# Optimization experiments

Measured on AMD Instinct MI355X. Metric: run time of the kernel, lower is better.

## Reference

```python
import jax, jax.numpy as jnp
import numpy as np

B, S = 1024, 256
E, EU = 8, 1            # total experts, universal experts
ES = E - EU             # specialized experts
UW = 0.3                # universal_expert_weight
NSTEPS = 1001
COV = 512
H = 128
DATA_DIM = 2


def setup_inputs() -> dict:
    key = jax.random.key(0)
    ks = iter(jax.random.split(key, 64))

    def nrm(shape, s=0.02):
        return jax.random.normal(next(ks), shape, jnp.float32) * s

    inp = {
        "y_t": jax.random.normal(next(ks), (B, S, 1), jnp.float32),
        "y_0_hat": jax.random.normal(next(ks), (B, S, 1), jnp.float32),
        "cov_embedding": jax.random.normal(next(ks), (B, COV), jnp.float32),
        "t": jax.random.randint(next(ks), (B,), 0, NSTEPS),
    }
    for l, nin in zip((1, 2, 3), (DATA_DIM, H, H)):
        inp[f"l{l}_emb"] = jax.random.uniform(next(ks), (NSTEPS, H), jnp.float32)  # embed.weight.uniform_()
        inp[f"l{l}_W"] = nrm((E, nin, H))      # per-expert Linear weights
        inp[f"l{l}_b"] = jnp.zeros((E, H), jnp.float32)
        inp[f"l{l}_Wc"] = nrm((COV, H))        # cov_projection
        inp[f"l{l}_bc"] = jnp.zeros((H,), jnp.float32)
        inp[f"l{l}_Wr1"] = nrm((COV, COV // 2))  # specialized_router layer 1
        inp[f"l{l}_br1"] = jnp.zeros((COV // 2,), jnp.float32)
        inp[f"l{l}_Wr2"] = nrm((COV // 2, ES))   # specialized_router layer 2
        inp[f"l{l}_br2"] = jnp.zeros((ES,), jnp.float32)
    inp["W4"] = nrm((H, 1))
    inp["b4"] = jnp.zeros((1,), jnp.float32)
    return inp


def _moe_layer(x, t, cov, emb, W, b, Wc, bc, Wr1, br1, Wr2, br2):
    # x: [B,S,in]; t: [B] int; cov: [B,COV]
    gamma = emb[t][:, None, :]                                   # [B,1,H]
    hr = jax.nn.relu(cov @ Wr1 + br1)                            # router (dropout inactive in eval)
    rw = jax.nn.softmax(hr @ Wr2 + br2, axis=-1) * (1.0 - UW)    # [B,ES] specialized routing weights
    w = jnp.concatenate(
        [jnp.full((x.shape[0], EU), UW / EU, x.dtype), rw], axis=1
    )                                                            # [B,E] full routing weights
    # gamma factors out of the weighted sum over experts, so fuse expert GEMMs + weighting:
    mix = jnp.einsum('bsi,eio,be->bso', x, W, w) + jnp.einsum('be,eo->bo', w, b)[:, None, :]
    mix = gamma * mix
    cov_gamma = cov @ Wc + bc                                    # [B,H]
    mix = mix * (1.0 + cov_gamma[:, None, :])
    usage = rw.mean(axis=0)                                      # mean over batch
    load = jnp.mean((usage - 1.0 / ES) ** 2)                     # mse vs uniform
    return mix, load


def reference(y_t, y_0_hat, cov_embedding, t,
              l1_emb, l1_W, l1_b, l1_Wc, l1_bc, l1_Wr1, l1_br1, l1_Wr2, l1_br2,
              l2_emb, l2_W, l2_b, l2_Wc, l2_bc, l2_Wr1, l2_br1, l2_Wr2, l2_br2,
              l3_emb, l3_W, l3_b, l3_Wc, l3_bc, l3_Wr1, l3_br1, l3_Wr2, l3_br2,
              W4, b4):
    h = jnp.concatenate([y_t, y_0_hat], axis=-1)                 # cat_y_pred: [B,S,2]
    h, ld1 = _moe_layer(h, t, cov_embedding, l1_emb, l1_W, l1_b, l1_Wc, l1_bc, l1_Wr1, l1_br1, l1_Wr2, l1_br2)
    h = jax.nn.softplus(h)
    h, ld2 = _moe_layer(h, t, cov_embedding, l2_emb, l2_W, l2_b, l2_Wc, l2_bc, l2_Wr1, l2_br1, l2_Wr2, l2_br2)
    h = jax.nn.softplus(h)
    h, ld3 = _moe_layer(h, t, cov_embedding, l3_emb, l3_W, l3_b, l3_Wc, l3_bc, l3_Wr1, l3_br1, l3_Wr2, l3_br2)
    h = jax.nn.softplus(h)
    out = h @ W4 + b4                                            # [B,S,1] velocity
    return out, ld1 + ld2 + ld3
```

## Files before the change

kernel.cpp:

```cpp
#include <hip/hip_runtime.h>
#include <hip/hip_bf16.h>
#include <math.h>

#define B_    1024
#define S_    256
#define COV_  512
#define H_    128
#define E_    8
#define ES_   7

#define W_WS_OFF   0
#define COVG_OFF   24576
#define USAGE_OFF  417792

#define AT_STRIDE  136
#define WT_STRIDE  40

typedef __attribute__((ext_vector_type(8))) short bf16x8;
typedef __attribute__((ext_vector_type(4))) float f32x4;

__device__ __forceinline__ float softplus_f(float x) {
    return fmaxf(x, 0.0f) + __logf(1.0f + __expf(-fabsf(x)));
}

__device__ __forceinline__ unsigned pk2_bf16(float a, float b) {
    __hip_bfloat162 h = __float22bfloat162_rn(make_float2(a, b));
    return *reinterpret_cast<unsigned*>(&h);
}
__device__ __forceinline__ void split_pair(float a, float b, unsigned &hi, unsigned &lo) {
    hi = pk2_bf16(a, b);
    float ha = __uint_as_float(hi << 16);
    float hb = __uint_as_float(hi & 0xffff0000u);
    lo = pk2_bf16(a - ha, b - hb);
}

struct RouterArgs {
    const float* cov;
    const float* Wr1[3];
    const float* br1[3];
    const float* Wr2[3];
    const float* br2[3];
    const float* Wc[3];
    const float* bc[3];
    float* ws;
};

__global__ __launch_bounds__(384) void router_kernel(RouterArgs a) {
    const int l   = blockIdx.y;
    const int b0  = blockIdx.x * 4;
    const int tid = threadIdx.x;

    __shared__ float4 covs[4][COV_ / 4];
    __shared__ float  hr[4][256];
    __shared__ float  susage[ES_];

    for (int f = tid; f < 512; f += 384) {
        const int bb = f >> 7, k4 = f & 127;
        covs[bb][k4] = ((const float4*)(a.cov + (size_t)(b0 + bb) * COV_))[k4];
    }
    if (tid < ES_) susage[tid] = 0.0f;
    __syncthreads();

    {
        const float* __restrict__ Wp;
        int stride; float bias;
        if (tid < 256) { Wp = a.Wr1[l] + tid;         stride = 256; bias = a.br1[l][tid]; }
        else           { Wp = a.Wc[l]  + (tid - 256); stride = 128; bias = a.bc[l][tid - 256]; }

        float acc[4] = {0.f, 0.f, 0.f, 0.f};
        #pragma unroll 4
        for (int k4 = 0; k4 < COV_ / 4; ++k4) {
            float w0 = Wp[(4 * k4 + 0) * stride];
            float w1 = Wp[(4 * k4 + 1) * stride];
            float w2 = Wp[(4 * k4 + 2) * stride];
            float w3 = Wp[(4 * k4 + 3) * stride];
            #pragma unroll
            for (int bb = 0; bb < 4; ++bb) {
                float4 c = covs[bb][k4];
                acc[bb] = fmaf(c.x, w0, acc[bb]);
                acc[bb] = fmaf(c.y, w1, acc[bb]);
                acc[bb] = fmaf(c.z, w2, acc[bb]);
                acc[bb] = fmaf(c.w, w3, acc[bb]);
            }
        }
        if (tid < 256) {
            #pragma unroll
            for (int bb = 0; bb < 4; ++bb)
                hr[bb][tid] = fmaxf(acc[bb] + bias, 0.0f);
        } else {
            #pragma unroll
            for (int bb = 0; bb < 4; ++bb)
                a.ws[COVG_OFF + (size_t)(l * B_ + b0 + bb) * H_ + (tid - 256)] = acc[bb] + bias;
        }
    }
    __syncthreads();

    {
        const int wave = tid >> 6;
        const int lane = tid & 63;
        if (wave < 4) {
            const int bb = wave;
            const int o = lane >> 3;
            const int g = lane & 7;
            float p = 0.0f;
            if (o < ES_) {
                #pragma unroll
                for (int m = 0; m < 32; ++m) {
                    const int k = g * 32 + m;
                    p = fmaf(hr[bb][k], a.Wr2[l][k * ES_ + o], p);
                }
            }
            p += __shfl_xor(p, 1);
            p += __shfl_xor(p, 2);
            p += __shfl_xor(p, 4);
            const float lg = p + ((o < ES_) ? a.br2[l][o] : 0.0f);
            float v[ES_];
            #pragma unroll
            for (int oo = 0; oo < ES_; ++oo) v[oo] = __shfl(lg, oo * 8, 64);
            if (lane == 0) {
                const int b = b0 + bb;
                float mx = v[0];
                #pragma unroll
                for (int oo = 1; oo < ES_; ++oo) mx = fmaxf(mx, v[oo]);
                float ex[ES_]; float s = 0.0f;
                #pragma unroll
                for (int oo = 0; oo < ES_; ++oo) { ex[oo] = __expf(v[oo] - mx); s += ex[oo]; }
                const float inv = 0.7f / s;
                float* wout = a.ws + W_WS_OFF + (size_t)(l * B_ + b) * 8;
                wout[0] = 0.3f;
                #pragma unroll
                for (int oo = 0; oo < ES_; ++oo) {
                    const float rwv = ex[oo] * inv;
                    wout[1 + oo] = rwv;
                    atomicAdd(&susage[oo], rwv);
                }
            }
        }
    }
    __syncthreads();
    if (tid < ES_) atomicAdd(a.ws + USAGE_OFF + l * ES_ + tid, susage[tid]);
}

struct MainArgs {
    const float* y_t;
    const float* y0;
    const int*   t;
    const float* emb[3];
    const float* W1;
    const float* W2;
    const float* W3;
    const float* b_[3];
    const float* W4;
    const float* b4;
    float* ws;
    float* out;
};

__global__ __launch_bounds__(512, 2) void main_kernel(MainArgs a) {
    __shared__ unsigned short Ahi[256 * AT_STRIDE];
    __shared__ unsigned short Alo[256 * AT_STRIDE];
    __shared__ unsigned short WtBuf[2][128 * WT_STRIDE];
    __shared__ float GPs[2][128];
    __shared__ float GPBs[2][128];
    __shared__ float W4s[128];

    const int tid  = threadIdx.x;
    const int b    = blockIdx.x;
    const int lane = tid & 63;
    const int w    = tid >> 6;
    const int wm   = w >> 1;
    const int wn   = w & 1;
    const int nl   = lane & 15;
    const int quad = lane >> 4;
    const int tb   = a.t[b];

    float* L1f = (float*)WtBuf;

    if (tid < 384) {
        const int l = tid >> 7, j = tid & 127;
        const float* wv = a.ws + W_WS_OFF + (size_t)(l * B_ + b) * 8;
        const float gamma = a.emb[l][tb * H_ + j];
        const float covg  = a.ws[COVG_OFF + (size_t)(l * B_ + b) * H_ + j];
        const float gp = gamma * (1.0f + covg);
        const float* bl = a.b_[l];
        float bm = 0.0f;
        #pragma unroll
        for (int e = 0; e < E_; ++e) bm = fmaf(wv[e], bl[e * H_ + j], bm);
        if (l == 0) {
            float s0 = 0.0f, s1 = 0.0f;
            #pragma unroll
            for (int e = 0; e < E_; ++e) {
                s0 = fmaf(wv[e], a.W1[e * 256 + j], s0);
                s1 = fmaf(wv[e], a.W1[e * 256 + 128 + j], s1);
            }
            L1f[j]       = gp * s0;
            L1f[128 + j] = gp * s1;
            L1f[256 + j] = gp * bm;
        } else {
            GPs[l - 1][j]  = gp;
            GPBs[l - 1][j] = gp * bm;
        }
    }
    if (tid < 128) W4s[tid] = a.W4[tid];
    __syncthreads();

    {
        const int tok = tid >> 1;
        const int jh  = (tid & 1) * 64;
        const float x0 = a.y_t[b * S_ + tok];
        const float x1 = a.y0[b * S_ + tok];
        #pragma unroll
        for (int g = 0; g < 8; ++g) {
            const int jb = jh + g * 8;
            unsigned hp[4], lp[4];
            #pragma unroll
            for (int p = 0; p < 4; ++p) {
                const int j0 = jb + 2 * p;
                float m0 = fmaf(x0, L1f[j0],     fmaf(x1, L1f[128 + j0],     L1f[256 + j0]));
                float m1 = fmaf(x0, L1f[j0 + 1], fmaf(x1, L1f[128 + j0 + 1], L1f[256 + j0 + 1]));
                split_pair(softplus_f(m0), softplus_f(m1), hp[p], lp[p]);
            }
            *(uint4*)&Ahi[tok * AT_STRIDE + jb] = make_uint4(hp[0], hp[1], hp[2], hp[3]);
            *(uint4*)&Alo[tok * AT_STRIDE + jb] = make_uint4(lp[0], lp[1], lp[2], lp[3]);
        }
    }

    const int bj  = tid & 127;
    const int bkg = tid >> 7;

    for (int L = 0; L < 2; ++L) {
        const float* __restrict__ Wg = L ? a.W3 : a.W2;
        const float* wv = a.ws + W_WS_OFF + (size_t)((L + 1) * B_ + b) * 8;
        float we[E_];
        #pragma unroll
        for (int e = 0; e < E_; ++e) we[e] = wv[e];

        f32x4 acc[4][4];
        #pragma unroll
        for (int mt = 0; mt < 4; ++mt)
            #pragma unroll
            for (int nt = 0; nt < 4; ++nt)
                acc[mt][nt] = (f32x4){0.f, 0.f, 0.f, 0.f};

        unsigned bh[4], blo_[4];
        auto build = [&](int kc) {
            float bacc[8] = {0,0,0,0,0,0,0,0};
            const float* base = Wg + (size_t)(kc * 32 + bkg * 8) * H_ + bj;
            #pragma unroll
            for (int e = 0; e < E_; ++e) {
                const float* p = base + (size_t)e * (H_ * H_);
                const float wE = we[e];
                #pragma unroll
                for (int i = 0; i < 8; ++i)
                    bacc[i] = fmaf(wE, p[i * H_], bacc[i]);
            }
            #pragma unroll
            for (int i = 0; i < 4; ++i)
                split_pair(bacc[2 * i], bacc[2 * i + 1], bh[i], blo_[i]);
        };

        build(0);

        for (int kc = 0; kc < 4; ++kc) {
            __syncthreads();
            *(uint4*)&WtBuf[0][bj * WT_STRIDE + bkg * 8] = make_uint4(bh[0], bh[1], bh[2], bh[3]);
            *(uint4*)&WtBuf[1][bj * WT_STRIDE + bkg * 8] = make_uint4(blo_[0], blo_[1], blo_[2], blo_[3]);
            __syncthreads();

            const int ka = kc * 32 + quad * 8;
            bf16x8 Af[4], Al[4], Bf[4], Bl[4];
            #pragma unroll
            for (int mt = 0; mt < 4; ++mt) {
                const int row = (wm * 64 + mt * 16 + nl) * AT_STRIDE + ka;
                Af[mt] = *(const bf16x8*)&Ahi[row];
                Al[mt] = *(const bf16x8*)&Alo[row];
            }
            #pragma unroll
            for (int nt = 0; nt < 4; ++nt) {
                const int row = (wn * 64 + nt * 16 + nl) * WT_STRIDE + quad * 8;
                Bf[nt] = *(const bf16x8*)&WtBuf[0][row];
                Bl[nt] = *(const bf16x8*)&WtBuf[1][row];
            }
            #pragma unroll
            for (int mt = 0; mt < 4; ++mt)
                #pragma unroll
                for (int nt = 0; nt < 4; ++nt) {
                    acc[mt][nt] = __builtin_amdgcn_mfma_f32_16x16x32_bf16(Af[mt], Bf[nt], acc[mt][nt], 0, 0, 0);
                    acc[mt][nt] = __builtin_amdgcn_mfma_f32_16x16x32_bf16(Af[mt], Bl[nt], acc[mt][nt], 0, 0, 0);
                    acc[mt][nt] = __builtin_amdgcn_mfma_f32_16x16x32_bf16(Al[mt], Bf[nt], acc[mt][nt], 0, 0, 0);
                }

            if (kc < 3) build(kc + 1);
        }
        __syncthreads();

        if (L == 0) {
            #pragma unroll
            for (int nt = 0; nt < 4; ++nt) {
                const int n = wn * 64 + nt * 16 + nl;
                const float gp = GPs[0][n], gpb = GPBs[0][n];
                #pragma unroll
                for (int mt = 0; mt < 4; ++mt) {
                    const int tok0 = wm * 64 + mt * 16 + quad * 4;
                    #pragma unroll
                    for (int rp = 0; rp < 2; ++rp) {
                        const float h0 = softplus_f(fmaf(gp, acc[mt][nt][2 * rp],     gpb));
                        const float h1 = softplus_f(fmaf(gp, acc[mt][nt][2 * rp + 1], gpb));
                        unsigned hh, ll;
                        split_pair(h0, h1, hh, ll);
                        const int t0 = tok0 + 2 * rp;
                        Ahi[t0 * AT_STRIDE + n]       = (unsigned short)hh;
                        Ahi[(t0 + 1) * AT_STRIDE + n] = (unsigned short)(hh >> 16);
                        Alo[t0 * AT_STRIDE + n]       = (unsigned short)ll;
                        Alo[(t0 + 1) * AT_STRIDE + n] = (unsigned short)(ll >> 16);
                    }
                }
            }
        } else {
            float po[4][4];
            #pragma unroll
            for (int mt = 0; mt < 4; ++mt)
                #pragma unroll
                for (int r = 0; r < 4; ++r) po[mt][r] = 0.0f;
            #pragma unroll
            for (int nt = 0; nt < 4; ++nt) {
                const int n = wn * 64 + nt * 16 + nl;
                const float gp = GPs[1][n], gpb = GPBs[1][n], w4 = W4s[n];
                #pragma unroll
                for (int mt = 0; mt < 4; ++mt)
                    #pragma unroll
                    for (int r = 0; r < 4; ++r) {
                        const float h = softplus_f(fmaf(gp, acc[mt][nt][r], gpb));
                        po[mt][r] = fmaf(h, w4, po[mt][r]);
                    }
            }
            #pragma unroll
            for (int mt = 0; mt < 4; ++mt)
                #pragma unroll
                for (int r = 0; r < 4; ++r) {
                    po[mt][r] += __shfl_xor(po[mt][r], 1);
                    po[mt][r] += __shfl_xor(po[mt][r], 2);
                    po[mt][r] += __shfl_xor(po[mt][r], 4);
                    po[mt][r] += __shfl_xor(po[mt][r], 8);
                }
            float* pos = (float*)WtBuf;
            if (nl == 0) {
                #pragma unroll
                for (int mt = 0; mt < 4; ++mt)
                    #pragma unroll
                    for (int r = 0; r < 4; ++r)
                        pos[(wm * 64 + mt * 16 + quad * 4 + r) * 2 + wn] = po[mt][r];
            }
            __syncthreads();
            if (tid < 256)
                a.out[b * S_ + tid] = pos[2 * tid] + pos[2 * tid + 1] + a.b4[0];
        }
    }

    if (b == 0 && tid == 0) {
        float ld = 0.0f;
        for (int l = 0; l < 3; ++l)
            for (int o = 0; o < ES_; ++o) {
                float u = a.ws[USAGE_OFF + l * ES_ + o] * (1.0f / (float)B_);
                float d = u - (1.0f / (float)ES_);
                ld = fmaf(d, d, ld);
            }
        a.out[B_ * S_] = ld * (1.0f / (float)ES_);
    }
}

extern "C" void kernel_launch(void* const* d_in, const int* in_sizes, int n_in,
                              void* d_out, int out_size, void* d_ws, size_t ws_size,
                              hipStream_t stream) {
    (void)in_sizes; (void)n_in; (void)out_size; (void)ws_size;

    RouterArgs ra;
    ra.cov = (const float*)d_in[2];
    ra.ws  = (float*)d_ws;

    MainArgs ma;
    ma.y_t = (const float*)d_in[0];
    ma.y0  = (const float*)d_in[1];
    ma.t   = (const int*)d_in[3];
    for (int l = 0; l < 3; ++l) {
        const int base = 4 + l * 9;
        ma.emb[l] = (const float*)d_in[base + 0];
        ma.b_[l]  = (const float*)d_in[base + 2];
        ra.Wc[l]  = (const float*)d_in[base + 3];
        ra.bc[l]  = (const float*)d_in[base + 4];
        ra.Wr1[l] = (const float*)d_in[base + 5];
        ra.br1[l] = (const float*)d_in[base + 6];
        ra.Wr2[l] = (const float*)d_in[base + 7];
        ra.br2[l] = (const float*)d_in[base + 8];
    }
    ma.W1 = (const float*)d_in[4 + 0 * 9 + 1];
    ma.W2 = (const float*)d_in[4 + 1 * 9 + 1];
    ma.W3 = (const float*)d_in[4 + 2 * 9 + 1];
    ma.W4 = (const float*)d_in[31];
    ma.b4 = (const float*)d_in[32];
    ma.ws  = (float*)d_ws;
    ma.out = (float*)d_out;

    (void)hipMemsetAsync((char*)d_ws + USAGE_OFF * sizeof(float), 0, 24 * sizeof(float), stream);
    router_kernel<<<dim3(256, 3, 1), 384, 0, stream>>>(ra);
    main_kernel<<<dim3(1024, 1, 1), 512, 0, stream>>>(ma);
}
```

Baseline: 322.5 us.

## Double main-kernel threads per block and read router cov directly

The main kernel now launches 1024 threads per block instead of 512. Each wave takes half as many token rows in the MFMA tiles, and the weight-build and layer-1 work are split more finely across threads. This aims to put more waves on each CU to hide latency, since LDS use already limits the kernel to about one block per CU. The launch bound of (1024, 4) may force a very low VGPR cap and cause register spills. Separately, the router kernel drops its shared-memory staging of the covariance rows and reads them directly from global memory inside the K loop, which removes one barrier but relies on caching for reuse.

```diff
diff --git a/kernel.cpp b/kernel.cpp
--- a/kernel.cpp
+++ b/kernel.cpp
@@ -50,16 +50,14 @@
     const int b0  = blockIdx.x * 4;
     const int tid = threadIdx.x;
 
-    __shared__ float4 covs[4][COV_ / 4];
-    __shared__ float  hr[4][256];
-    __shared__ float  susage[ES_];
-
-    for (int f = tid; f < 512; f += 384) {
-        const int bb = f >> 7, k4 = f & 127;
-        covs[bb][k4] = ((const float4*)(a.cov + (size_t)(b0 + bb) * COV_))[k4];
-    }
+    __shared__ float hr[4][256];
+    __shared__ float susage[ES_];
     if (tid < ES_) susage[tid] = 0.0f;
-    __syncthreads();
+
+    const float* __restrict__ c0 = a.cov + (size_t)(b0 + 0) * COV_;
+    const float* __restrict__ c1 = a.cov + (size_t)(b0 + 1) * COV_;
+    const float* __restrict__ c2 = a.cov + (size_t)(b0 + 2) * COV_;
+    const float* __restrict__ c3 = a.cov + (size_t)(b0 + 3) * COV_;
 
     {
         const float* __restrict__ Wp;
@@ -67,30 +65,26 @@
         if (tid < 256) { Wp = a.Wr1[l] + tid;         stride = 256; bias = a.br1[l][tid]; }
         else           { Wp = a.Wc[l]  + (tid - 256); stride = 128; bias = a.bc[l][tid - 256]; }
 
-        float acc[4] = {0.f, 0.f, 0.f, 0.f};
-        #pragma unroll 4
-        for (int k4 = 0; k4 < COV_ / 4; ++k4) {
-            float w0 = Wp[(4 * k4 + 0) * stride];
-            float w1 = Wp[(4 * k4 + 1) * stride];
-            float w2 = Wp[(4 * k4 + 2) * stride];
-            float w3 = Wp[(4 * k4 + 3) * stride];
-            #pragma unroll
-            for (int bb = 0; bb < 4; ++bb) {
-                float4 c = covs[bb][k4];
-                acc[bb] = fmaf(c.x, w0, acc[bb]);
-                acc[bb] = fmaf(c.y, w1, acc[bb]);
-                acc[bb] = fmaf(c.z, w2, acc[bb]);
-                acc[bb] = fmaf(c.w, w3, acc[bb]);
-            }
+        float acc0 = 0.f, acc1 = 0.f, acc2 = 0.f, acc3 = 0.f;
+        #pragma unroll 8
+        for (int k = 0; k < COV_; ++k) {
+            const float wv = Wp[(size_t)k * stride];
+            acc0 = fmaf(c0[k], wv, acc0);
+            acc1 = fmaf(c1[k], wv, acc1);
+            acc2 = fmaf(c2[k], wv, acc2);
+            acc3 = fmaf(c3[k], wv, acc3);
         }
         if (tid < 256) {
-            #pragma unroll
-            for (int bb = 0; bb < 4; ++bb)
-                hr[bb][tid] = fmaxf(acc[bb] + bias, 0.0f);
+            hr[0][tid] = fmaxf(acc0 + bias, 0.0f);
+            hr[1][tid] = fmaxf(acc1 + bias, 0.0f);
+            hr[2][tid] = fmaxf(acc2 + bias, 0.0f);
+            hr[3][tid] = fmaxf(acc3 + bias, 0.0f);
         } else {
-            #pragma unroll
-            for (int bb = 0; bb < 4; ++bb)
-                a.ws[COVG_OFF + (size_t)(l * B_ + b0 + bb) * H_ + (tid - 256)] = acc[bb] + bias;
+            const int j = tid - 256;
+            a.ws[COVG_OFF + (size_t)(l * B_ + b0 + 0) * H_ + j] = acc0 + bias;
+            a.ws[COVG_OFF + (size_t)(l * B_ + b0 + 1) * H_ + j] = acc1 + bias;
+            a.ws[COVG_OFF + (size_t)(l * B_ + b0 + 2) * H_ + j] = acc2 + bias;
+            a.ws[COVG_OFF + (size_t)(l * B_ + b0 + 3) * H_ + j] = acc3 + bias;
         }
     }
     __syncthreads();
@@ -156,7 +150,7 @@
     float* out;
 };
 
-__global__ __launch_bounds__(512, 2) void main_kernel(MainArgs a) {
+__global__ __launch_bounds__(1024, 4) void main_kernel(MainArgs a) {
     __shared__ unsigned short Ahi[256 * AT_STRIDE];
     __shared__ unsigned short Alo[256 * AT_STRIDE];
     __shared__ unsigned short WtBuf[2][128 * WT_STRIDE];
@@ -205,12 +199,12 @@
     __syncthreads();
 
     {
-        const int tok = tid >> 1;
-        const int jh  = (tid & 1) * 64;
+        const int tok = tid >> 2;
+        const int jh  = (tid & 3) * 32;
         const float x0 = a.y_t[b * S_ + tok];
         const float x1 = a.y0[b * S_ + tok];
         #pragma unroll
-        for (int g = 0; g < 8; ++g) {
+        for (int g = 0; g < 4; ++g) {
             const int jb = jh + g * 8;
             unsigned hp[4], lp[4];
             #pragma unroll
@@ -235,43 +229,42 @@
         #pragma unroll
         for (int e = 0; e < E_; ++e) we[e] = wv[e];
 
-        f32x4 acc[4][4];
+        f32x4 acc[2][4];
         #pragma unroll
-        for (int mt = 0; mt < 4; ++mt)
+        for (int mt = 0; mt < 2; ++mt)
             #pragma unroll
             for (int nt = 0; nt < 4; ++nt)
                 acc[mt][nt] = (f32x4){0.f, 0.f, 0.f, 0.f};
 
-        unsigned bh[4], blo_[4];
+        unsigned bh[2], blo_[2];
         auto build = [&](int kc) {
-            float bacc[8] = {0,0,0,0,0,0,0,0};
-            const float* base = Wg + (size_t)(kc * 32 + bkg * 8) * H_ + bj;
+            float bacc[4] = {0.f, 0.f, 0.f, 0.f};
+            const float* base = Wg + (size_t)(kc * 32 + bkg * 4) * H_ + bj;
             #pragma unroll
             for (int e = 0; e < E_; ++e) {
                 const float* p = base + (size_t)e * (H_ * H_);
                 const float wE = we[e];
                 #pragma unroll
-                for (int i = 0; i < 8; ++i)
+                for (int i = 0; i < 4; ++i)
                     bacc[i] = fmaf(wE, p[i * H_], bacc[i]);
             }
-            #pragma unroll
-            for (int i = 0; i < 4; ++i)
-                split_pair(bacc[2 * i], bacc[2 * i + 1], bh[i], blo_[i]);
+            split_pair(bacc[0], bacc[1], bh[0], blo_[0]);
+            split_pair(bacc[2], bacc[3], bh[1], blo_[1]);
         };
 
         build(0);
 
         for (int kc = 0; kc < 4; ++kc) {
             __syncthreads();
-            *(uint4*)&WtBuf[0][bj * WT_STRIDE + bkg * 8] = make_uint4(bh[0], bh[1], bh[2], bh[3]);
-            *(uint4*)&WtBuf[1][bj * WT_STRIDE + bkg * 8] = make_uint4(blo_[0], blo_[1], blo_[2], blo_[3]);
+            *(uint2*)&WtBuf[0][bj * WT_STRIDE + bkg * 4] = make_uint2(bh[0], bh[1]);
+            *(uint2*)&WtBuf[1][bj * WT_STRIDE + bkg * 4] = make_uint2(blo_[0], blo_[1]);
             __syncthreads();
 
             const int ka = kc * 32 + quad * 8;
-            bf16x8 Af[4], Al[4], Bf[4], Bl[4];
-            #pragma unroll
-            for (int mt = 0; mt < 4; ++mt) {
-                const int row = (wm * 64 + mt * 16 + nl) * AT_STRIDE + ka;
+            bf16x8 Af[2], Al[2], Bf[4], Bl[4];
+            #pragma unroll
+            for (int mt = 0; mt < 2; ++mt) {
+                const int row = (wm * 32 + mt * 16 + nl) * AT_STRIDE + ka;
                 Af[mt] = *(const bf16x8*)&Ahi[row];
                 Al[mt] = *(const bf16x8*)&Alo[row];
             }
@@ -282,7 +275,7 @@
                 Bl[nt] = *(const bf16x8*)&WtBuf[1][row];
             }
             #pragma unroll
-            for (int mt = 0; mt < 4; ++mt)
+            for (int mt = 0; mt < 2; ++mt)
                 #pragma unroll
                 for (int nt = 0; nt < 4; ++nt) {
                     acc[mt][nt] = __builtin_amdgcn_mfma_f32_16x16x32_bf16(Af[mt], Bf[nt], acc[mt][nt], 0, 0, 0);
@@ -300,8 +293,8 @@
                 const int n = wn * 64 + nt * 16 + nl;
                 const float gp = GPs[0][n], gpb = GPBs[0][n];
                 #pragma unroll
-                for (int mt = 0; mt < 4; ++mt) {
-                    const int tok0 = wm * 64 + mt * 16 + quad * 4;
+                for (int mt = 0; mt < 2; ++mt) {
+                    const int tok0 = wm * 32 + mt * 16 + quad * 4;
                     #pragma unroll
                     for (int rp = 0; rp < 2; ++rp) {
                         const float h0 = softplus_f(fmaf(gp, acc[mt][nt][2 * rp],     gpb));
@@ -317,9 +310,9 @@
                 }
             }
         } else {
-            float po[4][4];
-            #pragma unroll
-            for (int mt = 0; mt < 4; ++mt)
+            float po[2][4];
+            #pragma unroll
+            for (int mt = 0; mt < 2; ++mt)
                 #pragma unroll
                 for (int r = 0; r < 4; ++r) po[mt][r] = 0.0f;
             #pragma unroll
@@ -327,7 +320,7 @@
                 const int n = wn * 64 + nt * 16 + nl;
                 const float gp = GPs[1][n], gpb = GPBs[1][n], w4 = W4s[n];
                 #pragma unroll
-                for (int mt = 0; mt < 4; ++mt)
+                for (int mt = 0; mt < 2; ++mt)
                     #pragma unroll
                     for (int r = 0; r < 4; ++r) {
                         const float h = softplus_f(fmaf(gp, acc[mt][nt][r], gpb));
@@ -335,7 +328,7 @@
                     }
             }
             #pragma unroll
-            for (int mt = 0; mt < 4; ++mt)
+            for (int mt = 0; mt < 2; ++mt)
                 #pragma unroll
                 for (int r = 0; r < 4; ++r) {
                     po[mt][r] += __shfl_xor(po[mt][r], 1);
@@ -346,10 +339,10 @@
             float* pos = (float*)WtBuf;
             if (nl == 0) {
                 #pragma unroll
-                for (int mt = 0; mt < 4; ++mt)
+                for (int mt = 0; mt < 2; ++mt)
                     #pragma unroll
                     for (int r = 0; r < 4; ++r)
-                        pos[(wm * 64 + mt * 16 + quad * 4 + r) * 2 + wn] = po[mt][r];
+                        pos[(wm * 32 + mt * 16 + quad * 4 + r) * 2 + wn] = po[mt][r];
             }
             __syncthreads();
             if (tid < 256)
@@ -403,5 +396,5 @@
 
     (void)hipMemsetAsync((char*)d_ws + USAGE_OFF * sizeof(float), 0, 24 * sizeof(float), stream);
     router_kernel<<<dim3(256, 3, 1), 384, 0, stream>>>(ra);
-    main_kernel<<<dim3(1024, 1, 1), 512, 0, stream>>>(ma);
-}
+    main_kernel<<<dim3(1024, 1, 1), 1024, 0, stream>>>(ma);
+}
```

Result: faster. 287.7 us (-10.8%).
